# Kernel tuning notes

Hardware: AMD Instinct MI355X
Metric: run time of the kernel (lower is better)

## Reference

```python
import jax, jax.numpy as jnp
import numpy as np

N_NODES = 100000
N_EDGES = 1600000
D_IN = 128
D_OUT = 128
EPS = 1e-12  # F.normalize default eps


def setup_inputs() -> dict:
    key = jax.random.key(0)
    k1, k2, k3, k4, k5 = jax.random.split(key, 5)
    x = jax.random.normal(k1, (N_NODES, D_IN), dtype=jnp.float32)
    edge_index = jax.random.randint(k2, (2, N_EDGES), 0, N_NODES, dtype=jnp.int64)
    # PyG SAGEConv params: lin_l (neighbor path, with bias), lin_r (root path, no bias)
    s = 1.0 / np.sqrt(D_IN)
    W_l = jax.random.uniform(k3, (D_IN, D_OUT), jnp.float32, -s, s)
    b_l = jax.random.uniform(k4, (D_OUT,), jnp.float32, -s, s)
    W_r = jax.random.uniform(k5, (D_IN, D_OUT), jnp.float32, -s, s)
    return {"x": x, "edge_index": edge_index, "W_l": W_l, "b_l": b_l, "W_r": W_r}


def reference(x, edge_index, W_l, b_l, W_r):
    n = x.shape[0]
    src = edge_index[0]  # message source nodes (x_j)
    dst = edge_index[1]  # aggregation targets (i)
    # gather + mean scatter-reduce
    msg = x[src]                                            # [E, D_IN]
    summed = jax.ops.segment_sum(msg, dst, num_segments=n)  # [N, D_IN]
    cnt = jax.ops.segment_sum(jnp.ones((msg.shape[0],), x.dtype), dst, num_segments=n)
    mean = summed / jnp.maximum(cnt, 1.0)[:, None]
    # lin_l(mean) + lin_r(x), then row-wise L2 normalize
    out = mean @ W_l + b_l + x @ W_r                        # [N, D_OUT]
    norm = jnp.sqrt(jnp.sum(out * out, axis=-1, keepdims=True))
    return out / jnp.maximum(norm, EPS)
```

## Files before the change

kernel.cpp:

```cpp
#include <hip/hip_runtime.h>
#include <hip/hip_bf16.h>

#define N_NODES 100000
#define N_EDGES 1600000
#define D 128
#define TILES (N_NODES / 16)
#define WPB 8
#define NB2 782
#define NPB2 128
#define CAP 4096
#define EPB 8192
#define PBLK 196
#define CVTB 6250
#define PREPB 128

typedef __attribute__((ext_vector_type(4))) float f32x4;
typedef __attribute__((ext_vector_type(8))) short short8;
typedef __attribute__((ext_vector_type(4))) unsigned int u32x4;
typedef __attribute__((ext_vector_type(2))) unsigned int u32x2;

static __device__ __forceinline__ unsigned short f2bf(float f) {
  unsigned u = __float_as_uint(f);
  u += 0x7fffu + ((u >> 16) & 1u);
  return (unsigned short)(u >> 16);
}

static __device__ __forceinline__ void acc4(u32x2 u, float& a0, float& a1,
                                            float& a2, float& a3) {
  a0 += __uint_as_float(u[0] << 16);
  a1 += __uint_as_float(u[0] & 0xffff0000u);
  a2 += __uint_as_float(u[1] << 16);
  a3 += __uint_as_float(u[1] & 0xffff0000u);
}

__global__ __launch_bounds__(256) void cvtw_k(const float* __restrict__ x,
                                              unsigned* __restrict__ xh,
                                              const float* __restrict__ Wl,
                                              const float* __restrict__ Wr,
                                              unsigned short* __restrict__ wt_g) {
  int t = threadIdx.x;
  if (blockIdx.x < CVTB) {
    size_t i = (size_t)blockIdx.x * 256 + t;
    const f32x4* p = (const f32x4*)(x + i * 8);
    f32x4 v0 = p[0], v1 = p[1];
    u32x4 o;
    o[0] = ((unsigned)f2bf(v0[1]) << 16) | f2bf(v0[0]);
    o[1] = ((unsigned)f2bf(v0[3]) << 16) | f2bf(v0[2]);
    o[2] = ((unsigned)f2bf(v1[1]) << 16) | f2bf(v1[0]);
    o[3] = ((unsigned)f2bf(v1[3]) << 16) | f2bf(v1[2]);
    *(u32x4*)(xh + i * 4) = o;
    return;
  }
  int i = (blockIdx.x - CVTB) * 256 + t;
  int k = i >> 7, c = i & 127;
  float w = (k < 128) ? Wl[k * 128 + c] : Wr[(k - 128) * 128 + c];
  int phys = (k >> 3) ^ (c & 7);
  wt_g[c * 256 + (phys << 3) + (k & 7)] = f2bf(w);
}

__global__ __launch_bounds__(256) void p1h_k(const int* __restrict__ ei,
                                             int* __restrict__ hist) {
  __shared__ int bh[NB2];
  int t = threadIdx.x;
  for (int i = t; i < NB2; i += 256) bh[i] = 0;
  __syncthreads();
  int base = blockIdx.x * EPB;
  int end = min(base + EPB, N_EDGES);
  for (int i = base + t; i < end; i += 256)
    atomicAdd(&bh[ei[N_EDGES + i] >> 7], 1);
  __syncthreads();
  for (int i = t; i < NB2; i += 256) hist[blockIdx.x * NB2 + i] = bh[i];
}

__global__ __launch_bounds__(256) void scanb_k(int* __restrict__ hist,
                                               int* __restrict__ bcnt) {
  __shared__ int s[256];
  int b = blockIdx.x, t = threadIdx.x;
  int v = (t < PBLK) ? hist[t * NB2 + b] : 0;
  s[t] = v;
  __syncthreads();
  for (int o = 1; o < 256; o <<= 1) {
    int u = (t >= o) ? s[t - o] : 0;
    __syncthreads();
    s[t] += u;
    __syncthreads();
  }
  if (t < PBLK) hist[t * NB2 + b] = s[t] - v;
  if (t == 0) bcnt[b] = min(s[255], CAP);
}

__global__ __launch_bounds__(256) void p3c_k(const int* __restrict__ ei,
                                             const int* __restrict__ hist,
                                             unsigned* __restrict__ part) {
  __shared__ int lbase[NB2], lcur[NB2];
  int t = threadIdx.x, blk = blockIdx.x;
  for (int i = t; i < NB2; i += 256) {
    lbase[i] = hist[blk * NB2 + i];
    lcur[i] = 0;
  }
  __syncthreads();
  int base = blk * EPB;
  int end = min(base + EPB, N_EDGES);
  for (int i = base + t; i < end; i += 256) {
    int dst = ei[N_EDGES + i];
    int src = ei[i];
    int b = dst >> 7;
    int rel = lbase[b] + atomicAdd(&lcur[b], 1);
    if (rel < CAP)
      part[(size_t)b * CAP + rel] =
          ((unsigned)(dst & (NPB2 - 1)) << 17) | (unsigned)src;
  }
}

__global__ __launch_bounds__(512) void p4c_k(unsigned* __restrict__ part,
                                             const int* __restrict__ bcnt,
                                             int2* __restrict__ pd) {
  __shared__ unsigned s_codes[CAP];
  __shared__ int s_deg[NPB2], s_scan[NPB2], s_off[NPB2];
  int t = threadIdx.x, b = blockIdx.x;
  int ne = min(bcnt[b], CAP);
  unsigned* pp = part + (size_t)b * CAP;
  for (int i = t; i < ne; i += 512) s_codes[i] = pp[i];
  if (t < NPB2) s_deg[t] = 0;
  __syncthreads();
  for (int i = t; i < ne; i += 512) atomicAdd(&s_deg[s_codes[i] >> 17], 1);
  __syncthreads();
  if (t < NPB2) s_scan[t] = s_deg[t];
  __syncthreads();
  for (int o = 1; o < NPB2; o <<= 1) {
    int u = (t >= o && t < NPB2) ? s_scan[t - o] : 0;
    __syncthreads();
    if (t < NPB2) s_scan[t] += u;
    __syncthreads();
  }
  if (t < NPB2) {
    int deg = s_deg[t];
    int ex = s_scan[t] - deg;
    s_off[t] = ex;
    int node = b * NPB2 + t;
    if (node < N_NODES) {
      int2 v;
      v.x = b * CAP + ex;
      v.y = deg;
      pd[node] = v;
    }
  }
  __syncthreads();
  for (int i = t; i < ne; i += 512) {
    unsigned c = s_codes[i];
    int pos = atomicAdd(&s_off[c >> 17], 1);
    pp[pos] = c & 0x1FFFFu;
  }
}

__global__ __launch_bounds__(256) void gather2_k(const unsigned* __restrict__ xh,
                                                 const unsigned* __restrict__ csr,
                                                 const int2* __restrict__ pd,
                                                 unsigned* __restrict__ mh) {
  int wid = (blockIdx.x * 256 + threadIdx.x) >> 6;
  int lane = threadIdx.x & 63;
  int half = lane >> 5, lh = lane & 31;
  int node = wid * 2 + half;
  if (node >= N_NODES) return;
  int2 v = pd[node];
  int base = v.x;
  int deg = v.y;
  float a0 = 0.f, a1 = 0.f, a2 = 0.f, a3 = 0.f;
  float b0 = 0.f, b1 = 0.f, b2 = 0.f, b3 = 0.f;
  for (int c = 0; c < deg; c += 32) {
    int rem = deg - c;
    int n = min(32, rem);
    int eidx = (lh < rem) ? (int)csr[base + c + lh] : 0;
    int j = 0;
    for (; j + 7 < n; j += 8) {
      int s0 = __shfl(eidx, j, 32);
      int s1 = __shfl(eidx, j + 1, 32);
      int s2 = __shfl(eidx, j + 2, 32);
      int s3 = __shfl(eidx, j + 3, 32);
      int s4 = __shfl(eidx, j + 4, 32);
      int s5 = __shfl(eidx, j + 5, 32);
      int s6 = __shfl(eidx, j + 6, 32);
      int s7 = __shfl(eidx, j + 7, 32);
      u32x2 u0 = *(const u32x2*)(xh + (size_t)s0 * 64 + lh * 2);
      u32x2 u1 = *(const u32x2*)(xh + (size_t)s1 * 64 + lh * 2);
      u32x2 u2 = *(const u32x2*)(xh + (size_t)s2 * 64 + lh * 2);
      u32x2 u3 = *(const u32x2*)(xh + (size_t)s3 * 64 + lh * 2);
      u32x2 u4 = *(const u32x2*)(xh + (size_t)s4 * 64 + lh * 2);
      u32x2 u5 = *(const u32x2*)(xh + (size_t)s5 * 64 + lh * 2);
      u32x2 u6 = *(const u32x2*)(xh + (size_t)s6 * 64 + lh * 2);
      u32x2 u7 = *(const u32x2*)(xh + (size_t)s7 * 64 + lh * 2);
      acc4(u0, a0, a1, a2, a3);
      acc4(u1, b0, b1, b2, b3);
      acc4(u2, a0, a1, a2, a3);
      acc4(u3, b0, b1, b2, b3);
      acc4(u4, a0, a1, a2, a3);
      acc4(u5, b0, b1, b2, b3);
      acc4(u6, a0, a1, a2, a3);
      acc4(u7, b0, b1, b2, b3);
    }
    for (; j + 3 < n; j += 4) {
      int s0 = __shfl(eidx, j, 32);
      int s1 = __shfl(eidx, j + 1, 32);
      int s2 = __shfl(eidx, j + 2, 32);
      int s3 = __shfl(eidx, j + 3, 32);
      u32x2 u0 = *(const u32x2*)(xh + (size_t)s0 * 64 + lh * 2);
      u32x2 u1 = *(const u32x2*)(xh + (size_t)s1 * 64 + lh * 2);
      u32x2 u2 = *(const u32x2*)(xh + (size_t)s2 * 64 + lh * 2);
      u32x2 u3 = *(const u32x2*)(xh + (size_t)s3 * 64 + lh * 2);
      acc4(u0, a0, a1, a2, a3);
      acc4(u1, b0, b1, b2, b3);
      acc4(u2, a0, a1, a2, a3);
      acc4(u3, b0, b1, b2, b3);
    }
    for (; j < n; j++) {
      int s0 = __shfl(eidx, j, 32);
      u32x2 u0 = *(const u32x2*)(xh + (size_t)s0 * 64 + lh * 2);
      acc4(u0, a0, a1, a2, a3);
    }
  }
  float inv = 1.0f / fmaxf((float)deg, 1.0f);
  a0 = (a0 + b0) * inv;
  a1 = (a1 + b1) * inv;
  a2 = (a2 + b2) * inv;
  a3 = (a3 + b3) * inv;
  u32x2 o;
  o[0] = ((unsigned)f2bf(a1) << 16) | f2bf(a0);
  o[1] = ((unsigned)f2bf(a3) << 16) | f2bf(a2);
  *(u32x2*)(mh + (size_t)node * 64 + lh * 2) = o;
}

__global__ __launch_bounds__(512) void fused_k(
    const unsigned* __restrict__ xh, const unsigned* __restrict__ mh,
    const unsigned* __restrict__ wt_g, const float* __restrict__ bl,
    float* __restrict__ out) {
  __shared__ unsigned Wt[16384];

  int tid = threadIdx.x;
  {
    const u32x4* src = (const u32x4*)wt_g;
    u32x4* dst = (u32x4*)Wt;
    #pragma unroll
    for (int it = 0; it < 8; it++) dst[it * 512 + tid] = src[it * 512 + tid];
  }
  __syncthreads();

  int tile = blockIdx.x * WPB + (tid >> 6);
  if (tile >= TILES) return;
  int lane = tid & 63;
  int c0 = lane & 15;
  int g = lane >> 4;
  int row0 = tile * 16;
  const unsigned short* Wt16 = (const unsigned short*)Wt;

  f32x4 acc[8];
  #pragma unroll
  for (int ct = 0; ct < 8; ct++)
    for (int j = 0; j < 4; j++) acc[ct][j] = 0.0f;

  #pragma unroll
  for (int kf = 0; kf < 8; kf++) {
    int koff = (kf & 3) * 32 + g * 8;
    const unsigned short* a_src = (const unsigned short*)((kf < 4) ? mh : xh);
    short8 af = *(const short8*)(a_src + (size_t)(row0 + c0) * D + koff);
    #pragma unroll
    for (int ct = 0; ct < 8; ct++) {
      int c = ct * 16 + c0;
      short8 bf = *(const short8*)&Wt16[c * 256 + ((((kf << 2) + g) ^ (c & 7)) << 3)];
      acc[ct] = __builtin_amdgcn_mfma_f32_16x16x32_bf16(af, bf, acc[ct], 0, 0, 0);
    }
  }

  float ss[4] = {0.f, 0.f, 0.f, 0.f};
  #pragma unroll
  for (int ct = 0; ct < 8; ct++) {
    float bias = bl[ct * 16 + c0];
    #pragma unroll
    for (int j = 0; j < 4; j++) {
      float v = acc[ct][j] + bias;
      acc[ct][j] = v;
      ss[j] += v * v;
    }
  }
  #pragma unroll
  for (int j = 0; j < 4; j++) {
    float s = ss[j];
    s += __shfl_xor(s, 1);
    s += __shfl_xor(s, 2);
    s += __shfl_xor(s, 4);
    s += __shfl_xor(s, 8);
    ss[j] = 1.0f / fmaxf(sqrtf(s), 1e-12f);
  }
  #pragma unroll
  for (int ct = 0; ct < 8; ct++) {
    #pragma unroll
    for (int j = 0; j < 4; j++) {
      out[(size_t)(row0 + g * 4 + j) * D + ct * 16 + c0] = acc[ct][j] * ss[j];
    }
  }
}

extern "C" void kernel_launch(void* const* d_in, const int* in_sizes, int n_in,
                              void* d_out, int out_size, void* d_ws, size_t ws_size,
                              hipStream_t stream) {
  const float* x  = (const float*)d_in[0];
  const int*   ei = (const int*)d_in[1];
  const float* Wl = (const float*)d_in[2];
  const float* bl = (const float*)d_in[3];
  const float* Wr = (const float*)d_in[4];
  float* out = (float*)d_out;

  int* w = (int*)d_ws;
  int* hist = w;
  int* bcnt = w + 153600;
  int2* pd = (int2*)(w + 154400);
  unsigned* part = (unsigned*)(w + 354400);
  unsigned short* wt_g = (unsigned short*)(w + 3557472);
  const size_t XH_OFF = 3573856ULL * 4;
  const size_t MH_OFF = XH_OFF + (size_t)N_NODES * D * 2;
  unsigned* xh = (unsigned*)((char*)d_ws + XH_OFF);
  unsigned* mh = (unsigned*)((char*)d_ws + MH_OFF);

  cvtw_k<<<CVTB + PREPB, 256, 0, stream>>>(x, xh, Wl, Wr, wt_g);
  p1h_k<<<PBLK, 256, 0, stream>>>(ei, hist);
  scanb_k<<<NB2, 256, 0, stream>>>(hist, bcnt);
  p3c_k<<<PBLK, 256, 0, stream>>>(ei, hist, part);
  p4c_k<<<NB2, 512, 0, stream>>>(part, bcnt, pd);
  gather2_k<<<12500, 256, 0, stream>>>(xh, part, pd, mh);
  fused_k<<<(TILES + WPB - 1) / WPB, 512, 0, stream>>>(xh, mh, (const unsigned*)wt_g, bl, out);
}
```

Baseline: 142.5 us.

## Fuse preprocessing kernels into one cooperative kernel with grid syncs

Merges the conversion, histogram, scan, scatter and per-bucket sort kernels into a single cooperative launch of 782 blocks of 512 threads, separated by grid-wide barriers. This removes four kernel launch boundaries and lets the weight conversion and x conversion overlap with the histogram phase. In exchange every phase is limited to a fixed grid, the block size changes, and each grid.sync has its own cost; occupancy must also allow all 782 blocks to be co-resident.

```diff
diff --git a/kernel.cpp b/kernel.cpp
--- a/kernel.cpp
+++ b/kernel.cpp
@@ -1,5 +1,8 @@
 #include <hip/hip_runtime.h>
+#include <hip/hip_cooperative_groups.h>
 #include <hip/hip_bf16.h>
+
+namespace cg = cooperative_groups;
 
 #define N_NODES 100000
 #define N_EDGES 1600000
@@ -11,8 +14,7 @@
 #define CAP 4096
 #define EPB 8192
 #define PBLK 196
-#define CVTB 6250
-#define PREPB 128
+#define GRID_P 782
 
 typedef __attribute__((ext_vector_type(4))) float f32x4;
 typedef __attribute__((ext_vector_type(8))) short short8;
@@ -33,14 +35,18 @@
   a3 += __uint_as_float(u[1] & 0xffff0000u);
 }
 
-__global__ __launch_bounds__(256) void cvtw_k(const float* __restrict__ x,
-                                              unsigned* __restrict__ xh,
-                                              const float* __restrict__ Wl,
-                                              const float* __restrict__ Wr,
-                                              unsigned short* __restrict__ wt_g) {
-  int t = threadIdx.x;
-  if (blockIdx.x < CVTB) {
-    size_t i = (size_t)blockIdx.x * 256 + t;
+__global__ __launch_bounds__(512) void prep_k(
+    const float* __restrict__ x, unsigned* __restrict__ xh,
+    const int* __restrict__ ei, int* __restrict__ hist,
+    int* __restrict__ bcnt, int2* __restrict__ pd,
+    unsigned* __restrict__ part, const float* __restrict__ Wl,
+    const float* __restrict__ Wr, unsigned short* __restrict__ wt_g) {
+  __shared__ int sm[4096 + 512];
+  cg::grid_group grid = cg::this_grid();
+  int t = threadIdx.x, bid = blockIdx.x;
+
+  for (size_t i = (size_t)bid * 512 + t; i < 1600000ULL;
+       i += (size_t)GRID_P * 512) {
     const f32x4* p = (const f32x4*)(x + i * 8);
     f32x4 v0 = p[0], v1 = p[1];
     u32x4 o;
@@ -49,107 +55,102 @@
     o[2] = ((unsigned)f2bf(v1[1]) << 16) | f2bf(v1[0]);
     o[3] = ((unsigned)f2bf(v1[3]) << 16) | f2bf(v1[2]);
     *(u32x4*)(xh + i * 4) = o;
-    return;
-  }
-  int i = (blockIdx.x - CVTB) * 256 + t;
-  int k = i >> 7, c = i & 127;
-  float w = (k < 128) ? Wl[k * 128 + c] : Wr[(k - 128) * 128 + c];
-  int phys = (k >> 3) ^ (c & 7);
-  wt_g[c * 256 + (phys << 3) + (k & 7)] = f2bf(w);
-}
-
-__global__ __launch_bounds__(256) void p1h_k(const int* __restrict__ ei,
-                                             int* __restrict__ hist) {
-  __shared__ int bh[NB2];
-  int t = threadIdx.x;
-  for (int i = t; i < NB2; i += 256) bh[i] = 0;
-  __syncthreads();
-  int base = blockIdx.x * EPB;
-  int end = min(base + EPB, N_EDGES);
-  for (int i = base + t; i < end; i += 256)
-    atomicAdd(&bh[ei[N_EDGES + i] >> 7], 1);
-  __syncthreads();
-  for (int i = t; i < NB2; i += 256) hist[blockIdx.x * NB2 + i] = bh[i];
-}
-
-__global__ __launch_bounds__(256) void scanb_k(int* __restrict__ hist,
-                                               int* __restrict__ bcnt) {
-  __shared__ int s[256];
-  int b = blockIdx.x, t = threadIdx.x;
-  int v = (t < PBLK) ? hist[t * NB2 + b] : 0;
-  s[t] = v;
-  __syncthreads();
-  for (int o = 1; o < 256; o <<= 1) {
-    int u = (t >= o) ? s[t - o] : 0;
-    __syncthreads();
-    s[t] += u;
-    __syncthreads();
-  }
-  if (t < PBLK) hist[t * NB2 + b] = s[t] - v;
-  if (t == 0) bcnt[b] = min(s[255], CAP);
-}
-
-__global__ __launch_bounds__(256) void p3c_k(const int* __restrict__ ei,
-                                             const int* __restrict__ hist,
-                                             unsigned* __restrict__ part) {
-  __shared__ int lbase[NB2], lcur[NB2];
-  int t = threadIdx.x, blk = blockIdx.x;
-  for (int i = t; i < NB2; i += 256) {
-    lbase[i] = hist[blk * NB2 + i];
-    lcur[i] = 0;
-  }
-  __syncthreads();
-  int base = blk * EPB;
-  int end = min(base + EPB, N_EDGES);
-  for (int i = base + t; i < end; i += 256) {
-    int dst = ei[N_EDGES + i];
-    int src = ei[i];
-    int b = dst >> 7;
-    int rel = lbase[b] + atomicAdd(&lcur[b], 1);
-    if (rel < CAP)
-      part[(size_t)b * CAP + rel] =
-          ((unsigned)(dst & (NPB2 - 1)) << 17) | (unsigned)src;
-  }
-}
-
-__global__ __launch_bounds__(512) void p4c_k(unsigned* __restrict__ part,
-                                             const int* __restrict__ bcnt,
-                                             int2* __restrict__ pd) {
-  __shared__ unsigned s_codes[CAP];
-  __shared__ int s_deg[NPB2], s_scan[NPB2], s_off[NPB2];
-  int t = threadIdx.x, b = blockIdx.x;
-  int ne = min(bcnt[b], CAP);
-  unsigned* pp = part + (size_t)b * CAP;
-  for (int i = t; i < ne; i += 512) s_codes[i] = pp[i];
-  if (t < NPB2) s_deg[t] = 0;
-  __syncthreads();
-  for (int i = t; i < ne; i += 512) atomicAdd(&s_deg[s_codes[i] >> 17], 1);
-  __syncthreads();
-  if (t < NPB2) s_scan[t] = s_deg[t];
-  __syncthreads();
-  for (int o = 1; o < NPB2; o <<= 1) {
-    int u = (t >= o && t < NPB2) ? s_scan[t - o] : 0;
-    __syncthreads();
-    if (t < NPB2) s_scan[t] += u;
-    __syncthreads();
-  }
-  if (t < NPB2) {
-    int deg = s_deg[t];
-    int ex = s_scan[t] - deg;
-    s_off[t] = ex;
-    int node = b * NPB2 + t;
-    if (node < N_NODES) {
-      int2 v;
-      v.x = b * CAP + ex;
-      v.y = deg;
-      pd[node] = v;
-    }
-  }
-  __syncthreads();
-  for (int i = t; i < ne; i += 512) {
-    unsigned c = s_codes[i];
-    int pos = atomicAdd(&s_off[c >> 17], 1);
-    pp[pos] = c & 0x1FFFFu;
+  }
+  if (bid < PBLK) {
+    int* bh = sm;
+    for (int i = t; i < NB2; i += 512) bh[i] = 0;
+    __syncthreads();
+    int base = bid * EPB;
+    int end = min(base + EPB, N_EDGES);
+    for (int i = base + t; i < end; i += 512)
+      atomicAdd(&bh[ei[N_EDGES + i] >> 7], 1);
+    __syncthreads();
+    for (int i = t; i < NB2; i += 512) hist[bid * NB2 + i] = bh[i];
+  } else if (bid < PBLK + 64) {
+    int i = (bid - PBLK) * 512 + t;
+    int k = i >> 7, c = i & 127;
+    float w = (k < 128) ? Wl[k * 128 + c] : Wr[(k - 128) * 128 + c];
+    int phys = (k >> 3) ^ (c & 7);
+    wt_g[c * 256 + (phys << 3) + (k & 7)] = f2bf(w);
+  }
+  grid.sync();
+
+  {
+    int* s = sm;
+    int v = (t < PBLK) ? hist[t * NB2 + bid] : 0;
+    if (t < 256) s[t] = v;
+    __syncthreads();
+    for (int o = 1; o < 256; o <<= 1) {
+      int u = (t >= o && t < 256) ? s[t - o] : 0;
+      __syncthreads();
+      if (t < 256) s[t] += u;
+      __syncthreads();
+    }
+    if (t < PBLK) hist[t * NB2 + bid] = s[t] - v;
+    if (t == 0) bcnt[bid] = min(s[255], CAP);
+  }
+  grid.sync();
+
+  if (bid < PBLK) {
+    int* lbase = sm;
+    int* lcur = sm + 800;
+    for (int i = t; i < NB2; i += 512) {
+      lbase[i] = hist[bid * NB2 + i];
+      lcur[i] = 0;
+    }
+    __syncthreads();
+    int base = bid * EPB;
+    int end = min(base + EPB, N_EDGES);
+    for (int i = base + t; i < end; i += 512) {
+      int dst = ei[N_EDGES + i];
+      int src = ei[i];
+      int b = dst >> 7;
+      int rel = lbase[b] + atomicAdd(&lcur[b], 1);
+      if (rel < CAP)
+        part[(size_t)b * CAP + rel] =
+            ((unsigned)(dst & (NPB2 - 1)) << 17) | (unsigned)src;
+    }
+  }
+  grid.sync();
+
+  {
+    unsigned* s_codes = (unsigned*)sm;
+    int* s_deg = sm + 4096;
+    int* s_scan = sm + 4096 + 128;
+    int* s_off = sm + 4096 + 256;
+    int ne = min(bcnt[bid], CAP);
+    unsigned* pp = part + (size_t)bid * CAP;
+    for (int i = t; i < ne; i += 512) s_codes[i] = pp[i];
+    if (t < NPB2) s_deg[t] = 0;
+    __syncthreads();
+    for (int i = t; i < ne; i += 512) atomicAdd(&s_deg[s_codes[i] >> 17], 1);
+    __syncthreads();
+    if (t < NPB2) s_scan[t] = s_deg[t];
+    __syncthreads();
+    for (int o = 1; o < NPB2; o <<= 1) {
+      int u = (t >= o && t < NPB2) ? s_scan[t - o] : 0;
+      __syncthreads();
+      if (t < NPB2) s_scan[t] += u;
+      __syncthreads();
+    }
+    if (t < NPB2) {
+      int deg = s_deg[t];
+      int ex = s_scan[t] - deg;
+      s_off[t] = ex;
+      int node = bid * NPB2 + t;
+      if (node < N_NODES) {
+        int2 v;
+        v.x = bid * CAP + ex;
+        v.y = deg;
+        pd[node] = v;
+      }
+    }
+    __syncthreads();
+    for (int i = t; i < ne; i += 512) {
+      unsigned c = s_codes[i];
+      int pos = atomicAdd(&s_off[c >> 17], 1);
+      pp[pos] = c & 0x1FFFFu;
+    }
   }
 }
 
@@ -320,11 +321,11 @@
   unsigned* xh = (unsigned*)((char*)d_ws + XH_OFF);
   unsigned* mh = (unsigned*)((char*)d_ws + MH_OFF);
 
-  cvtw_k<<<CVTB + PREPB, 256, 0, stream>>>(x, xh, Wl, Wr, wt_g);
-  p1h_k<<<PBLK, 256, 0, stream>>>(ei, hist);
-  scanb_k<<<NB2, 256, 0, stream>>>(hist, bcnt);
-  p3c_k<<<PBLK, 256, 0, stream>>>(ei, hist, part);
-  p4c_k<<<NB2, 512, 0, stream>>>(part, bcnt, pd);
+  void* args[] = {(void*)&x,  (void*)&xh, (void*)&ei, (void*)&hist,
+                  (void*)&bcnt, (void*)&pd, (void*)&part, (void*)&Wl,
+                  (void*)&Wr, (void*)&wt_g};
+  hipLaunchCooperativeKernel(reinterpret_cast<void*>(prep_k), dim3(GRID_P),
+                             dim3(512), args, 0, stream);
   gather2_k<<<12500, 256, 0, stream>>>(xh, part, pd, mh);
   fused_k<<<(TILES + WPB - 1) / WPB, 512, 0, stream>>>(xh, mh, (const unsigned*)wt_g, bl, out);
 }
```

Result: slower. 420.6 us (+195.3%).
